# Performance work log

Measured on AMD Instinct MI355X. Metric: run time of the kernel, lower is better.

Reference implementation:

```python
import jax, jax.numpy as jnp
import numpy as np
from jax import lax

NC1, NC2, NC3 = 64, 64, 512
TEMP = 1.0
EPS = 1e-5
B = 256


def setup_inputs() -> dict:
    key = jax.random.key(0)
    ks = jax.random.split(key, 16)
    d = {}
    d["inp"] = jax.random.normal(ks[0], (B, 3, 32, 32), jnp.float32)
    d["conv1_w"] = jax.random.normal(ks[1], (6, 3, 5, 5), jnp.float32) * 0.1
    d["conv1_b"] = jax.random.normal(ks[2], (6,), jnp.float32) * 0.1
    d["bn1_g"] = jnp.ones((6,), jnp.float32)
    d["bn1_b"] = jnp.zeros((6,), jnp.float32)
    d["conv2_w"] = jax.random.normal(ks[3], (16, 6, 5, 5), jnp.float32) * 0.1
    d["conv2_b"] = jax.random.normal(ks[4], (16,), jnp.float32) * 0.1
    d["bn2_g"] = jnp.ones((16,), jnp.float32)
    d["bn2_b"] = jnp.zeros((16,), jnp.float32)
    d["fc1_w"] = jax.random.normal(ks[5], (120, 400), jnp.float32) * 0.05
    d["fc1_b"] = jax.random.normal(ks[6], (120,), jnp.float32) * 0.05
    d["fc2_w"] = jax.random.normal(ks[7], (10, 120), jnp.float32) * 0.05
    d["fc2_b"] = jax.random.normal(ks[8], (10,), jnp.float32) * 0.05
    d["k1s"] = jax.random.normal(ks[9], (NC1, 6), jnp.float32)
    d["k2s"] = jax.random.normal(ks[10], (NC2, 16), jnp.float32)
    d["k3s"] = jax.random.normal(ks[11], (NC3, 120), jnp.float32)
    return d


def _conv(x, w, b):
    y = lax.conv_general_dilated(x, w, (1, 1), 'VALID',
                                 dimension_numbers=('NCHW', 'OIHW', 'NCHW'))
    return y + b[None, :, None, None]


def _bn_train(x, g, b):
    # BatchNorm2d in training mode: biased batch stats over (N,H,W)
    mean = x.mean(axis=(0, 2, 3), keepdims=True)
    var = ((x - mean) ** 2).mean(axis=(0, 2, 3), keepdims=True)
    return (x - mean) / jnp.sqrt(var + EPS) * g[None, :, None, None] + b[None, :, None, None]


def _maxpool2(x):
    return lax.reduce_window(x, -jnp.inf, lax.max, (1, 1, 2, 2), (1, 1, 2, 2), 'VALID')


def _codebook_logits_spatial(act, keys):
    # act: [B,C,H,W], keys: [K,C] -> -||act - k||_2 over C -> [B,K,H,W]
    diff = act[:, None] - keys[None, :, :, None, None]
    return -jnp.sqrt((diff ** 2).sum(axis=2))


def _neural_gas_loss(v, temp):
    n_clusters = v.shape[1]
    weightings = jnp.exp(-jnp.arange(n_clusters, dtype=v.dtype) / temp)
    sorted_v = jnp.sort(v, axis=1)
    return (sorted_v ** 2 * weightings).sum(axis=1)


def reference(inp, conv1_w, conv1_b, bn1_g, bn1_b, conv2_w, conv2_b, bn2_g, bn2_b,
              fc1_w, fc1_b, fc2_w, fc2_b, k1s, k2s, k3s):
    act1 = _bn_train(_conv(inp, conv1_w, conv1_b), bn1_g, bn1_b)          # [B,6,28,28]
    act_logits1 = _codebook_logits_spatial(act1, k1s)                     # [B,NC1,28,28]
    x = _maxpool2(jax.nn.relu(act1))                                      # [B,6,14,14]
    act2 = _bn_train(_conv(x, conv2_w, conv2_b), bn2_g, bn2_b)            # [B,16,10,10]
    act_logits2 = _codebook_logits_spatial(act2, k2s)                     # [B,NC2,10,10]
    x = _maxpool2(jax.nn.relu(act2))                                      # [B,16,5,5]
    x = x.reshape(x.shape[0], -1)                                         # [B,400]
    act3 = x @ fc1_w.T + fc1_b                                            # [B,120]
    diff3 = act3[:, None, :] - k3s[None, :, :]
    act_logits3 = -jnp.sqrt((diff3 ** 2).sum(axis=2))                     # [B,NC3]
    x = jax.nn.relu(act3)
    act4 = x @ fc2_w.T + fc2_b                                            # [B,10]
    # ARGS.ng branch: neural-gas cluster loss + argmax assignments
    cluster_loss = _neural_gas_loss(act_logits3, TEMP)                    # [B]
    assignments = jnp.argmax(act_logits3, axis=1)                         # [B] int
    return (assignments, cluster_loss.mean(), act4, act_logits1, act_logits2, act_logits3)
```

## Files before the change

kernel.cpp:

```cpp
#include <hip/hip_runtime.h>

#define B 256
#define EPSV 1e-5f

#define OFF_ASSIGN 0
#define OFF_LOSS   256
#define OFF_ACT4   257
#define OFF_L1     2817
#define OFF_L2     12847873
#define OFF_L3     14486273

__device__ __forceinline__ void wave_reduce2(float& s, float& q) {
#pragma unroll
    for (int o = 32; o > 0; o >>= 1) {
        s += __shfl_down(s, o, 64);
        q += __shfl_down(q, o, 64);
    }
}

__global__ __launch_bounds__(256) void conv1_kernel(
        const float* __restrict__ inp, const float* __restrict__ w,
        const float* __restrict__ bias, float* __restrict__ c1,
        float* __restrict__ part,
        const float* __restrict__ w1, const float* __restrict__ k3,
        float* __restrict__ w1t, float* __restrict__ k3st) {
    int bc = blockIdx.x;
    int tid = threadIdx.x;
    if (bc >= 1536) {
        int idx = (bc - 1536) * 256 + tid;
        if (idx < 48000) {
            int c = idx / 120, o = idx % 120;
            w1t[idx] = w1[o * 400 + c];
        } else if (idx < 48000 + 61440) {
            int j = idx - 48000;
            int c = j >> 9, k = j & 511;
            k3st[j] = k3[k * 120 + c];
        }
        return;
    }
    int b = bc / 6, c = bc % 6;
    __shared__ float ws[75];
    __shared__ float rs[4], rq[4];
    if (tid < 75) ws[tid] = w[c * 75 + tid];
    __syncthreads();
    const float* ip = inp + b * 3072;
    float bs = bias[c];
    float s = 0.f, sq = 0.f;
    for (int hw = tid; hw < 784; hw += 256) {
        int oh = hw / 28, ow = hw % 28;
        float acc = bs;
#pragma unroll
        for (int ic = 0; ic < 3; ++ic) {
            const float* ipc = ip + ic * 1024 + oh * 32 + ow;
            const float* wc = ws + ic * 25;
#pragma unroll
            for (int kh = 0; kh < 5; ++kh)
#pragma unroll
                for (int kw = 0; kw < 5; ++kw)
                    acc += ipc[kh * 32 + kw] * wc[kh * 5 + kw];
        }
        c1[bc * 784 + hw] = acc;
        s += acc; sq += acc * acc;
    }
    wave_reduce2(s, sq);
    if ((tid & 63) == 0) { rs[tid >> 6] = s; rq[tid >> 6] = sq; }
    __syncthreads();
    if (tid == 0) {
        part[bc * 2]     = rs[0] + rs[1] + rs[2] + rs[3];
        part[bc * 2 + 1] = rq[0] + rq[1] + rq[2] + rq[3];
    }
}

__global__ __launch_bounds__(1024) void stage1_kernel(
        const float* __restrict__ c1raw, const float* __restrict__ part1,
        const float* __restrict__ g1, const float* __restrict__ bb1,
        const float* __restrict__ k1s,
        const float* __restrict__ c2w, const float* __restrict__ c2b,
        float* __restrict__ out, float* __restrict__ c2raw,
        float* __restrict__ part2) {
    int b = blockIdx.x, tid = threadIdx.x;
    int lane = tid & 63, wid = tid >> 6;
    __shared__ __align__(16) float act[4704];
    __shared__ float sk1[384], k2sq1[64];
    __shared__ float w2s[2400];
    __shared__ float xp[1176];
    __shared__ __align__(16) float sa[1600];
    __shared__ float chs[6], chq[6], ssc[6], ssh[6];
    if (wid < 6) {
        float s = 0.f, q = 0.f;
#pragma unroll
        for (int j = 0; j < 4; ++j) {
            int bi = lane + 64 * j;
            s += part1[(bi * 6 + wid) * 2];
            q += part1[(bi * 6 + wid) * 2 + 1];
        }
        wave_reduce2(s, q);
        if (lane == 0) { chs[wid] = s; chq[wid] = q; }
    }
    if (tid >= 640 && tid < 1024) sk1[tid - 640] = k1s[tid - 640];
    for (int i = tid; i < 2400; i += 1024) w2s[i] = c2w[i];
    __syncthreads();
    if (tid < 6) {
        float m = chs[tid] * (1.f / 200704.f);
        float v = chq[tid] * (1.f / 200704.f) - m * m;
        float sc = g1[tid] * rsqrtf(v + EPSV);
        ssc[tid] = sc; ssh[tid] = bb1[tid] - m * sc;
    }
    if (tid >= 64 && tid < 128) {
        int k = tid - 64;
        float s = 0.f;
#pragma unroll
        for (int c = 0; c < 6; ++c) { float x = sk1[k * 6 + c]; s += x * x; }
        k2sq1[k] = s;
    }
    __syncthreads();
    for (int i = tid; i < 4704; i += 1024) {
        int c = i / 784;
        act[i] = c1raw[b * 4704 + i] * ssc[c] + ssh[c];
    }
    __syncthreads();
    if (tid < 784) {
        float a0 = act[tid], a1 = act[784 + tid], a2 = act[1568 + tid];
        float a3 = act[2352 + tid], a4 = act[3136 + tid], a5 = act[3920 + tid];
        float A2 = a0*a0 + a1*a1 + a2*a2 + a3*a3 + a4*a4 + a5*a5;
        float* op = out + OFF_L1 + (long)b * 50176 + tid;
#pragma unroll 4
        for (int k = 0; k < 64; ++k) {
            const float* kp = sk1 + k * 6;
            float dot = a0*kp[0] + a1*kp[1] + a2*kp[2] + a3*kp[3] + a4*kp[4] + a5*kp[5];
            *op = -sqrtf(fmaxf(A2 + k2sq1[k] - 2.f * dot, 0.f));
            op += 784;
        }
    } else {
        for (int i = tid - 784; i < 1176; i += 240) {
            int c = i / 196, p = i % 196, ph = p / 14, pw = p % 14;
            const float* ap = act + c * 784 + ph * 56 + pw * 2;
            float m = fmaxf(fmaxf(ap[0], ap[1]), fmaxf(ap[28], ap[29]));
            xp[i] = fmaxf(m, 0.f);
        }
    }
    __syncthreads();
    for (int i = tid; i < 1600; i += 1024) {
        int c = i / 100, hw = i - c * 100;
        int oh = hw / 10, ow = hw - oh * 10;
        float acc = c2b[c];
#pragma unroll
        for (int ic = 0; ic < 6; ++ic) {
            const float* xsrc = xp + ic * 196 + oh * 14 + ow;
            const float* wp = w2s + c * 150 + ic * 25;
#pragma unroll
            for (int kh = 0; kh < 5; ++kh)
#pragma unroll
                for (int kw = 0; kw < 5; ++kw)
                    acc += xsrc[kh * 14 + kw] * wp[kh * 5 + kw];
        }
        sa[i] = acc;
        c2raw[b * 1600 + i] = acc;
    }
    __syncthreads();
    {
        float s = 0.f, q = 0.f;
        if (lane < 100) { float x = sa[wid * 100 + lane]; s = x; q = x * x; }
        if (lane < 36)  { float x = sa[wid * 100 + 64 + lane]; s += x; q += x * x; }
        wave_reduce2(s, q);
        if (lane == 0) { part2[(b * 16 + wid) * 2] = s; part2[(b * 16 + wid) * 2 + 1] = q; }
    }
}

__global__ __launch_bounds__(1024) void stage2_kernel(
        const float* __restrict__ c2raw, const float* __restrict__ part2,
        const float* __restrict__ g2, const float* __restrict__ bb2,
        const float* __restrict__ k2s,
        const float* __restrict__ w1t, const float* __restrict__ f1b,
        const float* __restrict__ f2w, const float* __restrict__ f2b,
        const float* __restrict__ k3st,
        float* __restrict__ out, float* __restrict__ lossb,
        unsigned* __restrict__ done) {
    int b = blockIdx.x, tid = threadIdx.x;
    int lane = tid & 63, wid = tid >> 6;
    __shared__ __align__(16) float sa[1600];
    __shared__ float sk2[1024], k2sq2[64];
    __shared__ float chs[16], chq[16], ssc[16], ssh[16];
    __shared__ float xs[400];
    __shared__ float partq[1024];
    __shared__ float a3r[120], a3p[120];
    __shared__ __align__(16) float sv[512];
    __shared__ __align__(16) float pv[1024];
    __shared__ int cntp[1024];
    __shared__ float wsum[8], wmv[8];
    __shared__ int wmi[8];
    __shared__ int lastflag;
    {
        float s = 0.f, q = 0.f;
#pragma unroll
        for (int j = 0; j < 4; ++j) {
            int bi = lane + 64 * j;
            s += part2[(bi * 16 + wid) * 2];
            q += part2[(bi * 16 + wid) * 2 + 1];
        }
        wave_reduce2(s, q);
        if (lane == 0) { chs[wid] = s; chq[wid] = q; }
    }
    sk2[tid] = k2s[tid];
    __syncthreads();
    if (tid < 16) {
        float m = chs[tid] * (1.f / 25600.f);
        float v = chq[tid] * (1.f / 25600.f) - m * m;
        float sc = g2[tid] * rsqrtf(v + EPSV);
        ssc[tid] = sc; ssh[tid] = bb2[tid] - m * sc;
    }
    if (tid >= 64 && tid < 128) {
        int k = tid - 64;
        float s = 0.f;
#pragma unroll
        for (int c = 0; c < 16; ++c) { float x = sk2[k * 16 + c]; s += x * x; }
        k2sq2[k] = s;
    }
    __syncthreads();
    for (int i = tid; i < 1600; i += 1024) {
        int c = i / 100;
        sa[i] = c2raw[b * 1600 + i] * ssc[c] + ssh[c];
    }
    __syncthreads();
    if (tid < 800) {
        int kg = tid / 100, hw = tid - kg * 100;
        float a[16], A2 = 0.f;
#pragma unroll
        for (int c = 0; c < 16; ++c) { a[c] = sa[c * 100 + hw]; A2 += a[c] * a[c]; }
        float* op2 = out + OFF_L2 + (long)b * 6400 + kg * 800 + hw;
#pragma unroll
        for (int k = kg * 8; k < kg * 8 + 8; ++k) {
            const float* kp = sk2 + k * 16;
            float dot = 0.f;
#pragma unroll
            for (int c = 0; c < 16; ++c) dot += a[c] * kp[c];
            *op2 = -sqrtf(fmaxf(A2 + k2sq2[k] - 2.f * dot, 0.f));
            op2 += 100;
        }
    } else {
        for (int i = tid - 800; i < 400; i += 224) {
            int c = i / 25, p = i % 25, ph = p / 5, pw = p % 5;
            const float* ap = sa + c * 100 + ph * 20 + pw * 2;
            float m = fmaxf(fmaxf(ap[0], ap[1]), fmaxf(ap[10], ap[11]));
            xs[i] = fmaxf(m, 0.f);
        }
    }
    __syncthreads();
    {
        int o = tid & 127, q8 = tid >> 7;
        float s = 0.f;
        if (o < 120) {
            const float* wp = w1t + (q8 * 50) * 120 + o;
            const float* xq = xs + q8 * 50;
#pragma unroll 10
            for (int c = 0; c < 50; ++c) s += xq[c] * wp[c * 120];
        }
        partq[q8 * 128 + o] = s;
    }
    __syncthreads();
    if (tid < 120) {
        float acc = f1b[tid];
#pragma unroll
        for (int q8 = 0; q8 < 8; ++q8) acc += partq[q8 * 128 + tid];
        a3r[tid] = acc;
        a3p[tid] = fmaxf(acc, 0.f);
    }
    __syncthreads();
    {
        int k = tid & 511, h = tid >> 9;
        const float* kp = k3st + k;
        float s = 0.f;
#pragma unroll 6
        for (int c = h * 60; c < h * 60 + 60; ++c) {
            float d = a3r[c] - kp[c * 512];
            s += d * d;
        }
        pv[h * 512 + k] = s;
    }
    if (tid < 10) {
        float acc = f2b[tid];
        const float* wp = f2w + tid * 120;
#pragma unroll 8
        for (int c = 0; c < 120; ++c) acc += a3p[c] * wp[c];
        out[OFF_ACT4 + b * 10 + tid] = acc;
    }
    __syncthreads();
    if (tid < 512) {
        float v = -sqrtf(pv[tid] + pv[512 + tid]);
        sv[tid] = v;
        out[OFF_L3 + (long)b * 512 + tid] = v;
    }
    __syncthreads();
    {
        int i = tid & 511, h = tid >> 9;
        float v = sv[i];
        const float4* sv4 = reinterpret_cast<const float4*>(sv);
        int cnt = 0;
#pragma unroll 8
        for (int j4 = h * 64; j4 < h * 64 + 64; ++j4) {
            float4 o4 = sv4[j4];
            int jb = j4 * 4;
            cnt += (o4.x < v || (o4.x == v && jb < i)) ? 1 : 0;
            cnt += (o4.y < v || (o4.y == v && jb + 1 < i)) ? 1 : 0;
            cnt += (o4.z < v || (o4.z == v && jb + 2 < i)) ? 1 : 0;
            cnt += (o4.w < v || (o4.w == v && jb + 3 < i)) ? 1 : 0;
        }
        cntp[h * 512 + i] = cnt;
    }
    __syncthreads();
    if (tid < 512) {
        float v = sv[tid];
        int cnt = cntp[tid] + cntp[512 + tid];
        float contrib = v * v * expf(-(float)cnt);
        float ssum = contrib;
#pragma unroll
        for (int o = 32; o > 0; o >>= 1) ssum += __shfl_down(ssum, o, 64);
        float mv = v; int mi = tid;
#pragma unroll
        for (int o = 32; o > 0; o >>= 1) {
            float ov = __shfl_down(mv, o, 64);
            int oi = __shfl_down(mi, o, 64);
            if (ov > mv || (ov == mv && oi < mi)) { mv = ov; mi = oi; }
        }
        if (lane == 0) { wsum[wid] = ssum; wmv[wid] = mv; wmi[wid] = mi; }
    }
    __syncthreads();
    if (tid == 0) {
        float tot = 0.f;
        float bmv = wmv[0]; int bmi = wmi[0];
#pragma unroll
        for (int w = 0; w < 8; ++w) {
            tot += wsum[w];
            if (wmv[w] > bmv || (wmv[w] == bmv && wmi[w] < bmi)) { bmv = wmv[w]; bmi = wmi[w]; }
        }
        lossb[b] = tot;
        out[OFF_ASSIGN + b] = (float)bmi;
        __threadfence();
        unsigned r = __hip_atomic_fetch_add(done, 1u, __ATOMIC_ACQ_REL, __HIP_MEMORY_SCOPE_AGENT);
        lastflag = (r == (unsigned)(gridDim.x - 1)) ? 1 : 0;
    }
    __syncthreads();
    if (lastflag) {
        float* rf = pv;
        if (tid < 256) rf[tid] = lossb[tid];
        __syncthreads();
        for (int s2 = 128; s2 > 0; s2 >>= 1) {
            if (tid < s2) rf[tid] += rf[tid + s2];
            __syncthreads();
        }
        if (tid == 0) out[OFF_LOSS] = rf[0] * (1.f / 256.f);
    }
}

extern "C" void kernel_launch(void* const* d_in, const int* in_sizes, int n_in,
                              void* d_out, int out_size, void* d_ws, size_t ws_size,
                              hipStream_t stream) {
    const float* inp = (const float*)d_in[0];
    const float* c1w = (const float*)d_in[1];
    const float* c1b = (const float*)d_in[2];
    const float* g1  = (const float*)d_in[3];
    const float* bb1 = (const float*)d_in[4];
    const float* c2w = (const float*)d_in[5];
    const float* c2b = (const float*)d_in[6];
    const float* g2  = (const float*)d_in[7];
    const float* bb2 = (const float*)d_in[8];
    const float* f1w = (const float*)d_in[9];
    const float* f1b = (const float*)d_in[10];
    const float* f2w = (const float*)d_in[11];
    const float* f2b = (const float*)d_in[12];
    const float* k1  = (const float*)d_in[13];
    const float* k2  = (const float*)d_in[14];
    const float* k3  = (const float*)d_in[15];
    float* out = (float*)d_out;

    float* W = (float*)d_ws;
    unsigned* done = (unsigned*)d_ws;
    float* part1 = W + 64;
    float* c1raw = W + 3136;
    float* c2raw = W + 1207360;
    float* part2 = W + 1616960;
    float* lossb = W + 1625152;
    float* w1t   = W + 1625408;
    float* k3st  = W + 1673408;

    hipMemsetAsync(d_ws, 0, 64, stream);
    conv1_kernel<<<1964, 256, 0, stream>>>(inp, c1w, c1b, c1raw, part1,
                                           f1w, k3, w1t, k3st);
    stage1_kernel<<<B, 1024, 0, stream>>>(c1raw, part1, g1, bb1, k1, c2w, c2b,
                                          out, c2raw, part2);
    stage2_kernel<<<B, 1024, 0, stream>>>(c2raw, part2, g2, bb2, k2,
                                          w1t, f1b, f2w, f2b, k3st, out, lossb, done);
}
```

Baseline: 103.3 us.

## Overlap conv2 with codebook logits and vectorize shared-memory key loads

Moves the pool1 computation before the layer-1 codebook logits so that the spare threads (784..943) can run conv2 concurrently with the logits instead of in a separate phase. Each conv2 thread now computes a full 10-wide output row and keeps input rows in registers for reuse. Keys for layer 1 are padded to 8 floats with the squared norm packed in, so they load as float4. Layer-2 keys and the fc1 inputs also get vectorized shared loads. The costs are an extra barrier and higher register pressure in the conv2 threads, and conv2 now rides alongside the store-heavy logits loop.

```diff
diff --git a/kernel.cpp b/kernel.cpp
--- a/kernel.cpp
+++ b/kernel.cpp
@@ -81,7 +81,7 @@
     int b = blockIdx.x, tid = threadIdx.x;
     int lane = tid & 63, wid = tid >> 6;
     __shared__ __align__(16) float act[4704];
-    __shared__ float sk1[384], k2sq1[64];
+    __shared__ __align__(16) float sk1p[512];
     __shared__ float w2s[2400];
     __shared__ float xp[1176];
     __shared__ __align__(16) float sa[1600];
@@ -97,7 +97,11 @@
         wave_reduce2(s, q);
         if (lane == 0) { chs[wid] = s; chq[wid] = q; }
     }
-    if (tid >= 640 && tid < 1024) sk1[tid - 640] = k1s[tid - 640];
+    if (tid >= 640 && tid < 1024) {
+        int idx = tid - 640;
+        int k = idx / 6, c = idx - k * 6;
+        sk1p[k * 8 + c] = k1s[idx];
+    }
     for (int i = tid; i < 2400; i += 1024) w2s[i] = c2w[i];
     __syncthreads();
     if (tid < 6) {
@@ -110,13 +114,21 @@
         int k = tid - 64;
         float s = 0.f;
 #pragma unroll
-        for (int c = 0; c < 6; ++c) { float x = sk1[k * 6 + c]; s += x * x; }
-        k2sq1[k] = s;
+        for (int c = 0; c < 6; ++c) { float x = sk1p[k * 8 + c]; s += x * x; }
+        sk1p[k * 8 + 6] = s;
+        sk1p[k * 8 + 7] = 0.f;
     }
     __syncthreads();
     for (int i = tid; i < 4704; i += 1024) {
         int c = i / 784;
         act[i] = c1raw[b * 4704 + i] * ssc[c] + ssh[c];
+    }
+    __syncthreads();
+    for (int i = tid; i < 1176; i += 1024) {
+        int c = i / 196, p = i % 196, ph = p / 14, pw = p % 14;
+        const float* ap = act + c * 784 + ph * 56 + pw * 2;
+        float m = fmaxf(fmaxf(ap[0], ap[1]), fmaxf(ap[28], ap[29]));
+        xp[i] = fmaxf(m, 0.f);
     }
     __syncthreads();
     if (tid < 784) {
@@ -126,36 +138,41 @@
         float* op = out + OFF_L1 + (long)b * 50176 + tid;
 #pragma unroll 4
         for (int k = 0; k < 64; ++k) {
-            const float* kp = sk1 + k * 6;
-            float dot = a0*kp[0] + a1*kp[1] + a2*kp[2] + a3*kp[3] + a4*kp[4] + a5*kp[5];
-            *op = -sqrtf(fmaxf(A2 + k2sq1[k] - 2.f * dot, 0.f));
+            const float4* kp4 = reinterpret_cast<const float4*>(sk1p + k * 8);
+            float4 kA = kp4[0], kB = kp4[1];
+            float dot = a0*kA.x + a1*kA.y + a2*kA.z + a3*kA.w + a4*kB.x + a5*kB.y;
+            *op = -sqrtf(fmaxf(A2 + kB.z - 2.f * dot, 0.f));
             op += 784;
         }
-    } else {
-        for (int i = tid - 784; i < 1176; i += 240) {
-            int c = i / 196, p = i % 196, ph = p / 14, pw = p % 14;
-            const float* ap = act + c * 784 + ph * 56 + pw * 2;
-            float m = fmaxf(fmaxf(ap[0], ap[1]), fmaxf(ap[28], ap[29]));
-            xp[i] = fmaxf(m, 0.f);
-        }
-    }
-    __syncthreads();
-    for (int i = tid; i < 1600; i += 1024) {
-        int c = i / 100, hw = i - c * 100;
-        int oh = hw / 10, ow = hw - oh * 10;
-        float acc = c2b[c];
-#pragma unroll
+    } else if (tid < 944) {
+        int j = tid - 784;
+        int c = j / 10, oh = j - c * 10;
+        float acc[10];
+        float bias2 = c2b[c];
+#pragma unroll
+        for (int ow = 0; ow < 10; ++ow) acc[ow] = bias2;
         for (int ic = 0; ic < 6; ++ic) {
-            const float* xsrc = xp + ic * 196 + oh * 14 + ow;
-            const float* wp = w2s + c * 150 + ic * 25;
-#pragma unroll
-            for (int kh = 0; kh < 5; ++kh)
-#pragma unroll
-                for (int kw = 0; kw < 5; ++kw)
-                    acc += xsrc[kh * 14 + kw] * wp[kh * 5 + kw];
-        }
-        sa[i] = acc;
-        c2raw[b * 1600 + i] = acc;
+            const float* xb = xp + ic * 196;
+            const float* wpc = w2s + c * 150 + ic * 25;
+#pragma unroll
+            for (int kh = 0; kh < 5; ++kh) {
+                const float* row = xb + (oh + kh) * 14;
+                float r[14];
+#pragma unroll
+                for (int t = 0; t < 14; ++t) r[t] = row[t];
+#pragma unroll
+                for (int kw = 0; kw < 5; ++kw) {
+                    float wgt = wpc[kh * 5 + kw];
+#pragma unroll
+                    for (int ow = 0; ow < 10; ++ow)
+                        acc[ow] += r[ow + kw] * wgt;
+                }
+            }
+        }
+        float* sp = sa + c * 100 + oh * 10;
+        float* gp = c2raw + b * 1600 + c * 100 + oh * 10;
+#pragma unroll
+        for (int ow = 0; ow < 10; ++ow) { sp[ow] = acc[ow]; gp[ow] = acc[ow]; }
     }
     __syncthreads();
     {
@@ -179,7 +196,8 @@
     int b = blockIdx.x, tid = threadIdx.x;
     int lane = tid & 63, wid = tid >> 6;
     __shared__ __align__(16) float sa[1600];
-    __shared__ float sk2[1024], k2sq2[64];
+    __shared__ __align__(16) float sk2[1024];
+    __shared__ float k2sq2[64];
     __shared__ float chs[16], chq[16], ssc[16], ssh[16];
     __shared__ float xs[400];
     __shared__ float partq[1024];
@@ -230,10 +248,12 @@
         float* op2 = out + OFF_L2 + (long)b * 6400 + kg * 800 + hw;
 #pragma unroll
         for (int k = kg * 8; k < kg * 8 + 8; ++k) {
-            const float* kp = sk2 + k * 16;
-            float dot = 0.f;
-#pragma unroll
-            for (int c = 0; c < 16; ++c) dot += a[c] * kp[c];
+            const float4* kp4 = reinterpret_cast<const float4*>(sk2 + k * 16);
+            float4 kA = kp4[0], kB = kp4[1], kC = kp4[2], kD = kp4[3];
+            float dot = a[0]*kA.x + a[1]*kA.y + a[2]*kA.z + a[3]*kA.w
+                      + a[4]*kB.x + a[5]*kB.y + a[6]*kB.z + a[7]*kB.w
+                      + a[8]*kC.x + a[9]*kC.y + a[10]*kC.z + a[11]*kC.w
+                      + a[12]*kD.x + a[13]*kD.y + a[14]*kD.z + a[15]*kD.w;
             *op2 = -sqrtf(fmaxf(A2 + k2sq2[k] - 2.f * dot, 0.f));
             op2 += 100;
         }
@@ -251,9 +271,12 @@
         float s = 0.f;
         if (o < 120) {
             const float* wp = w1t + (q8 * 50) * 120 + o;
-            const float* xq = xs + q8 * 50;
-#pragma unroll 10
-            for (int c = 0; c < 50; ++c) s += xq[c] * wp[c * 120];
+            const float2* xq = reinterpret_cast<const float2*>(xs + q8 * 50);
+#pragma unroll 5
+            for (int c2 = 0; c2 < 25; ++c2) {
+                float2 xv = xq[c2];
+                s += xv.x * wp[(2 * c2) * 120] + xv.y * wp[(2 * c2 + 1) * 120];
+            }
         }
         partq[q8 * 128 + o] = s;
     }
```

After: 98.49 us. 4.6% less time.
